# Optimization experiments

Measured on AMD Instinct MI355X. Metric: run time of the kernel, lower is better.

Reference implementation:

```python
import jax, jax.numpy as jnp
import numpy as np

B, L, D, H = 4, 2048, 1024, 16
DK = D // H
SCALE = 1.0 / (DK ** 0.5)


def setup_inputs() -> dict:
    key = jax.random.key(0)
    ks = jax.random.split(key, 7)
    std = 1.0 / np.sqrt(D)
    return {
        "q": jax.random.normal(ks[0], (B, L, D), jnp.float32),
        "k": jax.random.normal(ks[1], (B, L, D), jnp.float32),
        "v": jax.random.normal(ks[2], (B, L, D), jnp.float32),
        # torch nn.Linear weights: shape (out_features, in_features)
        "w_q": jax.random.normal(ks[3], (D, D), jnp.float32) * std,
        "w_k": jax.random.normal(ks[4], (D, D), jnp.float32) * std,
        "w_v": jax.random.normal(ks[5], (D, D), jnp.float32) * std,
        "w_o": jax.random.normal(ks[6], (D, D), jnp.float32) * std,
    }


def _split_heads(x):
    # (B, L, D) -> (B, H, L, DK)
    return x.reshape(B, L, H, DK).transpose(0, 2, 1, 3)


def reference(q, k, v, w_q, w_k, w_v, w_o):
    # Linear projections (no bias): y = x @ W^T
    qh = _split_heads(jnp.einsum('bld,ed->ble', q, w_q))
    kh = _split_heads(jnp.einsum('bld,ed->ble', k, w_k))
    vh = _split_heads(jnp.einsum('bld,ed->ble', v, w_v))
    # scaled dot-product attention; score is (B, H, L, L)
    score = jnp.einsum('bhqd,bhkd->bhqk', qh, kh) * SCALE
    probs = jax.nn.softmax(score, axis=-1)  # dropout p=0.0 -> identity
    attn = jnp.einsum('bhqk,bhkd->bhqd', probs, vh)
    # merge heads and output projection
    o = attn.transpose(0, 2, 1, 3).reshape(B, L, D)
    return jnp.einsum('bld,ed->ble', o, w_o)
```

## Files before the change

### kernel.cpp

```cpp
#include <hip/hip_runtime.h>
#include <stdint.h>

typedef unsigned short u16;
typedef __attribute__((ext_vector_type(8))) short short8;
typedef __attribute__((ext_vector_type(4))) float floatx4;

#define DEV __device__ __forceinline__

DEV u16 f2bf(float f) {
  union { float f; unsigned u; } x; x.f = f;
  unsigned u = x.u + 0x7fffu + ((x.u >> 16) & 1u);
  return (u16)(u >> 16);
}
DEV float scrub(float x) {
  return fminf(fmaxf(x, -65504.0f), 65504.0f);
}
DEV void async16(const void* g, void* l) {
  auto gp = reinterpret_cast<const __attribute__((address_space(1))) unsigned int*>(
      reinterpret_cast<uintptr_t>(g));
  auto lp = reinterpret_cast<__attribute__((address_space(3))) unsigned int*>(
      reinterpret_cast<uintptr_t>(l));
  __builtin_amdgcn_global_load_lds(gp, lp, 16, 0, 0);
}
DEV unsigned asu(float f) { union { float f; unsigned u; } x; x.f = f; return x.u; }
DEV float asf(unsigned u) { union { unsigned u; float f; } x; x.u = u; return x.f; }

__global__ void cvt7(const float* __restrict__ a, const float* __restrict__ b,
                     const float* __restrict__ c, const float* __restrict__ w0,
                     const float* __restrict__ w1, const float* __restrict__ w2,
                     const float* __restrict__ w3,
                     u16* __restrict__ oa, u16* __restrict__ ob, u16* __restrict__ oc,
                     u16* __restrict__ o0, u16* __restrict__ o1, u16* __restrict__ o2,
                     u16* __restrict__ o3,
                     int n4a, int n4w) {
  int z = blockIdx.z;
  const float* s;
  u16* d;
  int n4;
  switch (z) {
    case 0: s = a;  d = oa; n4 = n4a; break;
    case 1: s = b;  d = ob; n4 = n4a; break;
    case 2: s = c;  d = oc; n4 = n4a; break;
    case 3: s = w0; d = o0; n4 = n4w; break;
    case 4: s = w1; d = o1; n4 = n4w; break;
    case 5: s = w2; d = o2; n4 = n4w; break;
    default: s = w3; d = o3; n4 = n4w; break;
  }
  int i = blockIdx.x * 256 + threadIdx.x;
  if (i < n4) {
    float4 v = ((const float4*)s)[i];
    union { u16 h[4]; uint2 u; } o;
    o.h[0] = f2bf(v.x); o.h[1] = f2bf(v.y); o.h[2] = f2bf(v.z); o.h[3] = f2bf(v.w);
    ((uint2*)d)[i] = o.u;
  }
}

__global__ __launch_bounds__(256, 2) void proj3(
    const u16* __restrict__ Xq, const u16* __restrict__ Xk, const u16* __restrict__ Xv,
    const u16* __restrict__ Wq, const u16* __restrict__ Wk, const u16* __restrict__ Wv,
    u16* __restrict__ Oq, u16* __restrict__ Ok, u16* __restrict__ Ov)
{
  constexpr int K = 1024;
  constexpr float SC2 = 0.125f * 1.44269504088896f;
  int flat = blockIdx.x + 8 * (blockIdx.y + 64 * blockIdx.z);
  int swz = (flat & 7) * 192 + (flat >> 3);
  const int bx = swz & 7, by = (swz >> 3) & 63, z = swz >> 9;

  const u16* X = z == 0 ? Xq : (z == 1 ? Xk : Xv);
  const u16* W = z == 0 ? Wq : (z == 1 ? Wk : Wv);
  u16* Out = z == 0 ? Oq : (z == 1 ? Ok : Ov);

  const u16* A = (z < 2) ? W : X;
  const u16* Bp = (z < 2) ? X : W;
  const int m0 = (z < 2) ? bx * 128 : by * 128;
  const int n0 = (z < 2) ? by * 128 : bx * 128;

  const int tid = threadIdx.x;
  const int w = tid >> 6, lane = tid & 63;
  const int quad = lane >> 4, l16 = lane & 15;
  const int wm = (w & 1) * 64, wn = (w >> 1) * 64;

  __shared__ u16 SM[32768];

  auto stage = [&](int p, int k0) {
#pragma unroll
    for (int i = 0; i < 4; ++i) {
      int lin = i * 256 + tid;
      int r = lin >> 3, sp = lin & 7, s = sp ^ (r & 7);
      async16(A + (size_t)(m0 + r) * K + k0 + s * 8, &SM[p * 8192 + lin * 8]);
    }
#pragma unroll
    for (int i = 0; i < 4; ++i) {
      int lin = i * 256 + tid;
      int r = lin >> 3, sp = lin & 7, s = sp ^ (r & 7);
      async16(Bp + (size_t)(n0 + r) * K + k0 + s * 8, &SM[16384 + p * 8192 + lin * 8]);
    }
  };

  floatx4 acc[4][4];
#pragma unroll
  for (int i = 0; i < 4; ++i)
#pragma unroll
    for (int j = 0; j < 4; ++j) acc[i][j] = (floatx4)0.0f;

  stage(0, 0);
  asm volatile("s_waitcnt vmcnt(0)" ::: "memory");
  __syncthreads();

  for (int k0 = 0; k0 < K; k0 += 64) {
    const int p = (k0 >> 6) & 1;
    if (k0 + 64 < K) stage(p ^ 1, k0 + 64);
    const u16* Asp = &SM[p * 8192];
    const u16* Bsp = &SM[16384 + p * 8192];

    __builtin_amdgcn_s_setprio(1);
#pragma unroll
    for (int kk = 0; kk < 2; ++kk) {
      short8 af[4], bf[4];
#pragma unroll
      for (int mi = 0; mi < 4; ++mi) {
        int r = wm + mi * 16 + l16;
        af[mi] = *(const short8*)&Asp[r * 64 + (((kk * 4 + quad) ^ (r & 7)) * 8)];
      }
#pragma unroll
      for (int ni = 0; ni < 4; ++ni) {
        int r = wn + ni * 16 + l16;
        bf[ni] = *(const short8*)&Bsp[r * 64 + (((kk * 4 + quad) ^ (r & 7)) * 8)];
      }
#pragma unroll
      for (int mi = 0; mi < 4; ++mi)
#pragma unroll
        for (int ni = 0; ni < 4; ++ni)
          acc[mi][ni] = __builtin_amdgcn_mfma_f32_16x16x32_bf16(af[mi], bf[ni], acc[mi][ni], 0, 0, 0);
    }
    __builtin_amdgcn_s_setprio(0);

    asm volatile("s_waitcnt vmcnt(0)" ::: "memory");
    __syncthreads();
  }

  const float sc = (z == 0) ? SC2 : 1.0f;
#pragma unroll
  for (int mi = 0; mi < 4; ++mi) {
#pragma unroll
    for (int ni = 0; ni < 4; ++ni) {
      int rr = m0 + wm + mi * 16 + quad * 4;
      int cc = n0 + wn + ni * 16 + l16;
      u16 h0 = f2bf(sc * acc[mi][ni][0]);
      u16 h1 = f2bf(sc * acc[mi][ni][1]);
      u16 h2 = f2bf(sc * acc[mi][ni][2]);
      u16 h3 = f2bf(sc * acc[mi][ni][3]);
      uint2 dw; dw.x = h0 | ((unsigned)h1 << 16); dw.y = h2 | ((unsigned)h3 << 16);
      if (z < 2) {
        int bb = cc >> 11, ll = cc & 2047;
        int hh = rr >> 6, dk0 = rr & 63;
        *(uint2*)&Out[(((size_t)bb * 16 + hh) * 2048 + ll) * 64 + dk0] = dw;
      } else {
        int bb = rr >> 11, ll0 = rr & 2047;
        int hh = cc >> 6, dk = cc & 63;
        *(uint2*)&Out[(((size_t)bb * 16 + hh) * 64 + dk) * 2048 + ll0] = dw;
      }
    }
  }
}

__global__ __launch_bounds__(256, 2) void gemm_out(
    const u16* __restrict__ Ah, const u16* __restrict__ Wo, float* __restrict__ Out)
{
  constexpr int K = 1024;
  const int tid = threadIdx.x;
  const int w = tid >> 6, lane = tid & 63;
  const int quad = lane >> 4, l16 = lane & 15;
  int flat = blockIdx.x + 8 * blockIdx.y;
  int swz = (flat & 7) * 64 + (flat >> 3);
  const int bx = swz & 7, by = swz >> 3;
  const int m0 = by * 128, n0 = bx * 128;
  const int wm = (w & 1) * 64, wn = (w >> 1) * 64;

  __shared__ u16 SM[32768];

  auto stage = [&](int p, int k0) {
#pragma unroll
    for (int i = 0; i < 4; ++i) {
      int lin = i * 256 + tid;
      int r = lin >> 3, sp = lin & 7, s = sp ^ (r & 7);
      int row = m0 + r;
      const u16* ga = Ah + (((size_t)(row >> 11) * 16 + (k0 >> 6)) * 2048 + (row & 2047)) * 64 + s * 8;
      async16(ga, &SM[p * 8192 + lin * 8]);
    }
#pragma unroll
    for (int i = 0; i < 4; ++i) {
      int lin = i * 256 + tid;
      int r = lin >> 3, sp = lin & 7, s = sp ^ (r & 7);
      async16(Wo + (size_t)(n0 + r) * K + k0 + s * 8, &SM[16384 + p * 8192 + lin * 8]);
    }
  };

  floatx4 acc[4][4];
#pragma unroll
  for (int i = 0; i < 4; ++i)
#pragma unroll
    for (int j = 0; j < 4; ++j) acc[i][j] = (floatx4)0.0f;

  stage(0, 0);
  asm volatile("s_waitcnt vmcnt(0)" ::: "memory");
  __syncthreads();

  for (int k0 = 0; k0 < K; k0 += 64) {
    const int p = (k0 >> 6) & 1;
    if (k0 + 64 < K) stage(p ^ 1, k0 + 64);
    const u16* Asp = &SM[p * 8192];
    const u16* Bsp = &SM[16384 + p * 8192];

    __builtin_amdgcn_s_setprio(1);
#pragma unroll
    for (int kk = 0; kk < 2; ++kk) {
      short8 af[4], bf[4];
#pragma unroll
      for (int mi = 0; mi < 4; ++mi) {
        int r = wm + mi * 16 + l16;
        af[mi] = *(const short8*)&Asp[r * 64 + (((kk * 4 + quad) ^ (r & 7)) * 8)];
      }
#pragma unroll
      for (int ni = 0; ni < 4; ++ni) {
        int r = wn + ni * 16 + l16;
        bf[ni] = *(const short8*)&Bsp[r * 64 + (((kk * 4 + quad) ^ (r & 7)) * 8)];
      }
#pragma unroll
      for (int mi = 0; mi < 4; ++mi)
#pragma unroll
        for (int ni = 0; ni < 4; ++ni)
          acc[mi][ni] = __builtin_amdgcn_mfma_f32_16x16x32_bf16(af[mi], bf[ni], acc[mi][ni], 0, 0, 0);
    }
    __builtin_amdgcn_s_setprio(0);

    asm volatile("s_waitcnt vmcnt(0)" ::: "memory");
    __syncthreads();
  }

#pragma unroll
  for (int mi = 0; mi < 4; ++mi)
#pragma unroll
    for (int ni = 0; ni < 4; ++ni) {
      int rr = m0 + wm + mi * 16 + quad * 4;
      int cc = n0 + wn + ni * 16 + l16;
#pragma unroll
      for (int reg = 0; reg < 4; ++reg)
        Out[(size_t)(rr + reg) * 1024 + cc] = scrub(acc[mi][ni][reg]);
    }
}

__global__ __launch_bounds__(256, 4) void attn3(
    const u16* Qh, const u16* __restrict__ Kh,
    const u16* __restrict__ VT, u16* O)
{
  constexpr int L = 2048, DK = 64, H = 16;
  const int tid = threadIdx.x;
  const int w = tid >> 6, lane = tid & 63;
  const int quad = lane >> 4, l16 = lane & 15;
  int flat = blockIdx.x + 16 * (blockIdx.y + 16 * blockIdx.z);
  int swz = (flat & 7) * 128 + (flat >> 3);
  const int q0 = (swz & 15) * 128;
  const int bh = swz >> 4;

  __shared__ u16 SM[4 * 64 * 64];
  u16* const QP = &SM[8192];
  char* const SMb = (char*)&SM[0];

  const u16* Qg = Qh + ((size_t)bh * L + q0) * DK;
  const u16* Kb = Kh + (size_t)bh * L * DK;
  const u16* Vb = VT + (size_t)bh * DK * L;

#pragma unroll
  for (int i = 0; i < 4; ++i) {
    int lin = i * 256 + tid;
    int r = lin >> 3, sp = lin & 7, s = sp ^ (r & 7);
    async16(Qg + (size_t)r * DK + s * 8, &QP[lin * 8]);
  }

  const int rA = tid >> 3;
  const int sA = (tid & 7) ^ (rA & 7);
  const u16* kg0 = Kb + (size_t)rA * DK + sA * 8;
  const u16* kg1 = kg0 + 32 * DK;
  const u16* vg0 = Vb + (size_t)rA * L + sA * 8;
  const u16* vg1 = vg0 + (size_t)32 * L;
  u16* const ldsB0 = &SM[tid * 8];
  u16* const ldsB1 = &SM[8192 + tid * 8];

  async16(kg0, ldsB0);
  async16(kg1, ldsB0 + 2048);
  async16(vg0, ldsB0 + 4096);
  async16(vg1, ldsB0 + 6144);
  kg0 += 64 * DK; kg1 += 64 * DK; vg0 += 64; vg1 += 64;

  asm volatile("s_waitcnt vmcnt(0)" ::: "memory");
  __syncthreads();

  short8 qf[2][2];
#pragma unroll
  for (int mi = 0; mi < 2; ++mi)
#pragma unroll
    for (int kk = 0; kk < 2; ++kk) {
      int r = w * 32 + mi * 16 + l16;
      qf[mi][kk] = *(const short8*)&QP[r * 64 + (((kk * 4 + quad) ^ (r & 7)) * 8)];
    }
  asm volatile("s_waitcnt lgkmcnt(0)" ::: "memory");
  __syncthreads();

  const int l7 = l16 & 7, qh2 = quad >> 1, qo = (quad & 1) * 8;
  int ka[2], vo[4];
#pragma unroll
  for (int kk = 0; kk < 2; ++kk)
    ka[kk] = l16 * 128 + (((kk * 4 + quad) ^ l7) * 16);
#pragma unroll
  for (int j = 0; j < 4; ++j)
    vo[j] = l16 * 128 + (((qh2 + 2 * j) ^ l7) * 16) + qo;

  short8 onesv;
#pragma unroll
  for (int j = 0; j < 8; ++j) onesv[j] = (short)0x3F80;

  floatx4 oT[4][2];
  floatx4 lacc[2];
#pragma unroll
  for (int nd = 0; nd < 4; ++nd)
#pragma unroll
    for (int mi = 0; mi < 2; ++mi) oT[nd][mi] = (floatx4)0.0f;
  lacc[0] = (floatx4)0.0f;
  lacc[1] = (floatx4)0.0f;

  auto body = [&](int PB, u16* ldsN, bool more) {
    if (more) {
      async16(kg0, ldsN);
      async16(kg1, ldsN + 2048);
      async16(vg0, ldsN + 4096);
      async16(vg1, ldsN + 6144);
      kg0 += 64 * DK; kg1 += 64 * DK; vg0 += 64; vg1 += 64;
    }

    floatx4 sT[4][2];
#pragma unroll
    for (int t = 0; t < 4; ++t)
#pragma unroll
      for (int mi = 0; mi < 2; ++mi) sT[t][mi] = (floatx4)0.0f;
    __builtin_amdgcn_s_setprio(1);
#pragma unroll
    for (int kk = 0; kk < 2; ++kk)
#pragma unroll
      for (int t = 0; t < 4; ++t) {
        short8 kf = *(const short8*)(SMb + PB + t * 2048 + ka[kk]);
#pragma unroll
        for (int mi = 0; mi < 2; ++mi)
          sT[t][mi] = __builtin_amdgcn_mfma_f32_16x16x32_bf16(kf, qf[mi][kk], sT[t][mi], 0, 0, 0);
      }
    __builtin_amdgcn_s_setprio(0);

#pragma unroll
    for (int t = 0; t < 4; ++t)
#pragma unroll
      for (int mi = 0; mi < 2; ++mi)
#pragma unroll
        for (int r = 0; r < 4; ++r) sT[t][mi][r] = __builtin_amdgcn_exp2f(sT[t][mi][r]);

    short8 pf[2][2];
#pragma unroll
    for (int g = 0; g < 2; ++g)
#pragma unroll
      for (int mi = 0; mi < 2; ++mi) {
        union { unsigned u[4]; short8 v; } up;
        up.u[0] = __builtin_amdgcn_perm(asu(sT[2 * g][mi][1]), asu(sT[2 * g][mi][0]), 0x07060302u);
        up.u[1] = __builtin_amdgcn_perm(asu(sT[2 * g][mi][3]), asu(sT[2 * g][mi][2]), 0x07060302u);
        up.u[2] = __builtin_amdgcn_perm(asu(sT[2 * g + 1][mi][1]), asu(sT[2 * g + 1][mi][0]), 0x07060302u);
        up.u[3] = __builtin_amdgcn_perm(asu(sT[2 * g + 1][mi][3]), asu(sT[2 * g + 1][mi][2]), 0x07060302u);
        pf[g][mi] = up.v;
      }

    __builtin_amdgcn_s_setprio(1);
#pragma unroll
    for (int g = 0; g < 2; ++g) {
#pragma unroll
      for (int nd = 0; nd < 4; ++nd) {
        union { uint2 ab[2]; short8 v; } uv;
        uv.ab[0] = *(const uint2*)(SMb + PB + 8192 + nd * 2048 + vo[2 * g]);
        uv.ab[1] = *(const uint2*)(SMb + PB + 8192 + nd * 2048 + vo[2 * g + 1]);
#pragma unroll
        for (int mi = 0; mi < 2; ++mi)
          oT[nd][mi] = __builtin_amdgcn_mfma_f32_16x16x32_bf16(uv.v, pf[g][mi], oT[nd][mi], 0, 0, 0);
      }
#pragma unroll
      for (int mi = 0; mi < 2; ++mi)
        lacc[mi] = __builtin_amdgcn_mfma_f32_16x16x32_bf16(onesv, pf[g][mi], lacc[mi], 0, 0, 0);
    }
    __builtin_amdgcn_s_setprio(0);

    asm volatile("s_waitcnt vmcnt(0)" ::: "memory");
    __syncthreads();
  };

  for (int j0 = 0; j0 < L; j0 += 128) {
    asm volatile("" : "+v"(ka[0]), "+v"(ka[1]),
                      "+v"(vo[0]), "+v"(vo[1]), "+v"(vo[2]), "+v"(vo[3]));
    body(0, ldsB1, true);
    body(16384, ldsB0, j0 + 128 < L);
  }

#pragma unroll
  for (int mi = 0; mi < 2; ++mi) {
    float inv = 1.0f / fmaxf(lacc[mi][0], 1e-30f);
    int token = q0 + w * 32 + mi * 16 + l16;
#pragma unroll
    for (int nd = 0; nd < 4; ++nd) {
      u16 h0 = f2bf(scrub(oT[nd][mi][0] * inv));
      u16 h1 = f2bf(scrub(oT[nd][mi][1] * inv));
      u16 h2 = f2bf(scrub(oT[nd][mi][2] * inv));
      u16 h3 = f2bf(scrub(oT[nd][mi][3] * inv));
      uint2 dw; dw.x = h0 | ((unsigned)h1 << 16); dw.y = h2 | ((unsigned)h3 << 16);
      *(uint2*)&O[((size_t)bh * L + token) * 64 + nd * 16 + quad * 4] = dw;
    }
  }
}

extern "C" void kernel_launch(void* const* d_in, const int* in_sizes, int n_in,
                              void* d_out, int out_size, void* d_ws, size_t ws_size,
                              hipStream_t stream) {
  const float* q  = (const float*)d_in[0];
  const float* k  = (const float*)d_in[1];
  const float* v  = (const float*)d_in[2];
  const float* wq = (const float*)d_in[3];
  const float* wk = (const float*)d_in[4];
  const float* wv = (const float*)d_in[5];
  const float* wo = (const float*)d_in[6];
  float* out = (float*)d_out;

  const size_t NE = (size_t)4 * 16 * 2048 * 64;
  const size_t WN = (size_t)1024 * 1024;

  u16* qb  = (u16*)d_ws;
  u16* kb  = qb + NE;
  u16* vb  = kb + NE;
  u16* wqb = vb + NE;
  u16* wkb = wqb + WN;
  u16* wvb = wkb + WN;
  u16* wob = wvb + WN;
  u16* Qh  = wob + WN;
  u16* Kh  = (u16*)d_out;
  u16* VTg = Kh + NE;

  int n4a = (int)(NE / 4), n4w = (int)(WN / 4);
  cvt7<<<dim3((n4a + 255) / 256, 1, 7), 256, 0, stream>>>(
      q, k, v, wq, wk, wv, wo, qb, kb, vb, wqb, wkb, wvb, wob, n4a, n4w);

  dim3 g1(8, 64, 3);
  proj3<<<g1, dim3(256), 0, stream>>>(qb, kb, vb, wqb, wkb, wvb, Qh, Kh, VTg);

  dim3 g2(16, 16, 4);
  attn3<<<g2, dim3(256), 0, stream>>>(Qh, Kh, VTg, Qh);

  dim3 g3(8, 64, 1);
  gemm_out<<<g3, dim3(256), 0, stream>>>(Qh, wob, out);
}
```

Before: 315.9 us.

## Flatten conversion grid and single-buffer projection GEMM for higher occupancy

The fp32-to-bf16 conversion kernel now uses a flat 1-D grid sized exactly to the work. Previously it ran a 7-deep z-grid in which the four weight slices launched mostly idle blocks. The projection GEMM drops LDS double-buffering, using 32 KB instead of 64 KB per block, and raises launch bounds from 2 to 4 blocks per CU. It also removes the s_setprio hints. This trades load/compute overlap within a block for more resident blocks hiding latency, and adds a barrier before compute in every k-step.

After: 305.5 us. -3.3%, faster.

```diff
diff --git a/kernel.cpp b/kernel.cpp
--- a/kernel.cpp
+++ b/kernel.cpp
@@ -31,31 +31,32 @@
                      const float* __restrict__ w3,
                      u16* __restrict__ oa, u16* __restrict__ ob, u16* __restrict__ oc,
                      u16* __restrict__ o0, u16* __restrict__ o1, u16* __restrict__ o2,
-                     u16* __restrict__ o3,
-                     int n4a, int n4w) {
-  int z = blockIdx.z;
+                     u16* __restrict__ o3) {
+  constexpr int N4A = 1 << 21;
+  constexpr int N4W = 1 << 18;
+  int i4 = blockIdx.x * 256 + threadIdx.x;
   const float* s;
   u16* d;
-  int n4;
-  switch (z) {
-    case 0: s = a;  d = oa; n4 = n4a; break;
-    case 1: s = b;  d = ob; n4 = n4a; break;
-    case 2: s = c;  d = oc; n4 = n4a; break;
-    case 3: s = w0; d = o0; n4 = n4w; break;
-    case 4: s = w1; d = o1; n4 = n4w; break;
-    case 5: s = w2; d = o2; n4 = n4w; break;
-    default: s = w3; d = o3; n4 = n4w; break;
-  }
-  int i = blockIdx.x * 256 + threadIdx.x;
-  if (i < n4) {
-    float4 v = ((const float4*)s)[i];
-    union { u16 h[4]; uint2 u; } o;
-    o.h[0] = f2bf(v.x); o.h[1] = f2bf(v.y); o.h[2] = f2bf(v.z); o.h[3] = f2bf(v.w);
-    ((uint2*)d)[i] = o.u;
-  }
-}
-
-__global__ __launch_bounds__(256, 2) void proj3(
+  int off;
+  if (i4 < 3 * N4A) {
+    int z = i4 >> 21;
+    off = i4 & (N4A - 1);
+    s = z == 0 ? a : (z == 1 ? b : c);
+    d = z == 0 ? oa : (z == 1 ? ob : oc);
+  } else {
+    int j = i4 - 3 * N4A;
+    int z = j >> 18;
+    off = j & (N4W - 1);
+    s = z == 0 ? w0 : (z == 1 ? w1 : (z == 2 ? w2 : w3));
+    d = z == 0 ? o0 : (z == 1 ? o1 : (z == 2 ? o2 : o3));
+  }
+  float4 v = ((const float4*)s)[off];
+  union { u16 h[4]; uint2 u; } o;
+  o.h[0] = f2bf(v.x); o.h[1] = f2bf(v.y); o.h[2] = f2bf(v.z); o.h[3] = f2bf(v.w);
+  ((uint2*)d)[off] = o.u;
+}
+
+__global__ __launch_bounds__(256, 4) void proj3(
     const u16* __restrict__ Xq, const u16* __restrict__ Xk, const u16* __restrict__ Xv,
     const u16* __restrict__ Wq, const u16* __restrict__ Wk, const u16* __restrict__ Wv,
     u16* __restrict__ Oq, u16* __restrict__ Ok, u16* __restrict__ Ov)
@@ -80,52 +81,43 @@
   const int quad = lane >> 4, l16 = lane & 15;
   const int wm = (w & 1) * 64, wn = (w >> 1) * 64;
 
-  __shared__ u16 SM[32768];
-
-  auto stage = [&](int p, int k0) {
+  __shared__ u16 As[128 * 64];
+  __shared__ u16 Bs[128 * 64];
+
+  floatx4 acc[4][4];
+#pragma unroll
+  for (int i = 0; i < 4; ++i)
+#pragma unroll
+    for (int j = 0; j < 4; ++j) acc[i][j] = (floatx4)0.0f;
+
+  for (int k0 = 0; k0 < K; k0 += 64) {
 #pragma unroll
     for (int i = 0; i < 4; ++i) {
       int lin = i * 256 + tid;
       int r = lin >> 3, sp = lin & 7, s = sp ^ (r & 7);
-      async16(A + (size_t)(m0 + r) * K + k0 + s * 8, &SM[p * 8192 + lin * 8]);
+      async16(A + (size_t)(m0 + r) * K + k0 + s * 8, &As[lin * 8]);
     }
 #pragma unroll
     for (int i = 0; i < 4; ++i) {
       int lin = i * 256 + tid;
       int r = lin >> 3, sp = lin & 7, s = sp ^ (r & 7);
-      async16(Bp + (size_t)(n0 + r) * K + k0 + s * 8, &SM[16384 + p * 8192 + lin * 8]);
-    }
-  };
-
-  floatx4 acc[4][4];
-#pragma unroll
-  for (int i = 0; i < 4; ++i)
-#pragma unroll
-    for (int j = 0; j < 4; ++j) acc[i][j] = (floatx4)0.0f;
-
-  stage(0, 0);
-  asm volatile("s_waitcnt vmcnt(0)" ::: "memory");
-  __syncthreads();
-
-  for (int k0 = 0; k0 < K; k0 += 64) {
-    const int p = (k0 >> 6) & 1;
-    if (k0 + 64 < K) stage(p ^ 1, k0 + 64);
-    const u16* Asp = &SM[p * 8192];
-    const u16* Bsp = &SM[16384 + p * 8192];
-
-    __builtin_amdgcn_s_setprio(1);
+      async16(Bp + (size_t)(n0 + r) * K + k0 + s * 8, &Bs[lin * 8]);
+    }
+    asm volatile("s_waitcnt vmcnt(0)" ::: "memory");
+    __syncthreads();
+
 #pragma unroll
     for (int kk = 0; kk < 2; ++kk) {
       short8 af[4], bf[4];
 #pragma unroll
       for (int mi = 0; mi < 4; ++mi) {
         int r = wm + mi * 16 + l16;
-        af[mi] = *(const short8*)&Asp[r * 64 + (((kk * 4 + quad) ^ (r & 7)) * 8)];
+        af[mi] = *(const short8*)&As[r * 64 + (((kk * 4 + quad) ^ (r & 7)) * 8)];
       }
 #pragma unroll
       for (int ni = 0; ni < 4; ++ni) {
         int r = wn + ni * 16 + l16;
-        bf[ni] = *(const short8*)&Bsp[r * 64 + (((kk * 4 + quad) ^ (r & 7)) * 8)];
+        bf[ni] = *(const short8*)&Bs[r * 64 + (((kk * 4 + quad) ^ (r & 7)) * 8)];
       }
 #pragma unroll
       for (int mi = 0; mi < 4; ++mi)
@@ -133,9 +125,6 @@
         for (int ni = 0; ni < 4; ++ni)
           acc[mi][ni] = __builtin_amdgcn_mfma_f32_16x16x32_bf16(af[mi], bf[ni], acc[mi][ni], 0, 0, 0);
     }
-    __builtin_amdgcn_s_setprio(0);
-
-    asm volatile("s_waitcnt vmcnt(0)" ::: "memory");
     __syncthreads();
   }
 
@@ -446,9 +435,8 @@
   u16* Kh  = (u16*)d_out;
   u16* VTg = Kh + NE;
 
-  int n4a = (int)(NE / 4), n4w = (int)(WN / 4);
-  cvt7<<<dim3((n4a + 255) / 256, 1, 7), 256, 0, stream>>>(
-      q, k, v, wq, wk, wv, wo, qb, kb, vb, wqb, wkb, wvb, wob, n4a, n4w);
+  cvt7<<<dim3(28672), 256, 0, stream>>>(
+      q, k, v, wq, wk, wv, wo, qb, kb, vb, wqb, wkb, wvb, wob);
 
   dim3 g1(8, 64, 3);
   proj3<<<g1, dim3(256), 0, stream>>>(qb, kb, vb, wqb, wkb, wvb, Qh, Kh, VTg);
```
